# Performance work log

Hardware: AMD Instinct MI355X
Metric: run time of the kernel (lower is better)

The kernel has to match this reference:

```python
import jax, jax.numpy as jnp
import numpy as np

N_NODES = 50000
N_EDGES = 400000
NODE_DIM = 128
NUM_BASIS = 20
MUL0, MUL1, MUL2 = 128, 64, 32          # 128x0e + 64x1e + 32x2e
NUM_IRREPS = MUL0 + MUL1 + MUL2         # 224
SPH_DIM = MUL0 + 3 * MUL1 + 5 * MUL2    # 480
HIDDEN = NODE_DIM + NUM_IRREPS          # 352
EPS = 1e-5


def layer_norm(x, g, b):
    mu = x.mean(-1, keepdims=True)
    var = ((x - mu) ** 2).mean(-1, keepdims=True)
    return (x - mu) * jax.lax.rsqrt(var + EPS) * g + b


def o3_layer_norm(x, w, b):
    # Equivariant layer norm per irrep block (Equiformer-style, component normalization).
    s = x[:, :MUL0]                                    # l=0 scalars [N,128]
    v = x[:, MUL0:MUL0 + 3 * MUL1].reshape(-1, MUL1, 3)  # l=1 [N,64,3]
    t = x[:, MUL0 + 3 * MUL1:].reshape(-1, MUL2, 5)      # l=2 [N,32,5]
    s = s - s.mean(-1, keepdims=True)
    s = s * jax.lax.rsqrt((s ** 2).mean(-1, keepdims=True) + EPS) * w[:MUL0] + b
    nv = (v ** 2).mean(axis=(-1, -2))[:, None, None]
    v = v * jax.lax.rsqrt(nv + EPS) * w[MUL0:MUL0 + MUL1][None, :, None]
    nt = (t ** 2).mean(axis=(-1, -2))[:, None, None]
    t = t * jax.lax.rsqrt(nt + EPS) * w[MUL0 + MUL1:][None, :, None]
    return jnp.concatenate([s, v.reshape(-1, 3 * MUL1), t.reshape(-1, 5 * MUL2)], axis=-1)


def sph_harm(vec):
    # e3nn spherical harmonics (normalize=True, normalization='component') up to l=2.
    u = vec * jax.lax.rsqrt((vec ** 2).sum(-1, keepdims=True))
    x, y, z = u[:, 0], u[:, 1], u[:, 2]
    s15 = np.float32(np.sqrt(15.0))
    s5 = np.float32(np.sqrt(5.0))
    sh1 = np.float32(np.sqrt(3.0)) * u  # [E,3]
    sh2 = jnp.stack([s15 * x * z,
                     s15 * x * y,
                     s5 * (y * y - 0.5 * (x * x + z * z)),
                     s15 * y * z,
                     0.5 * s15 * (z * z - x * x)], axis=-1)  # [E,5]
    return sh1, sh2


def _forward(x_scalar, x_spherical, rbf, vec, W1, b1, W2, b2, Wrbf, ln_g, ln_b, o3_w, o3_b, edge_index):
    dst, src = edge_index[0], edge_index[1]
    scalar_in = layer_norm(x_scalar, ln_g, ln_b)          # [N,128]
    spherical_in = o3_layer_norm(x_spherical, o3_w, o3_b)  # [N,480]
    h = jax.nn.silu(scalar_in @ W1 + b1)
    scalar_out = h @ W2 + b2                               # [N,352]
    filter_weight = rbf @ Wrbf                             # [E,352]
    filter_out = scalar_out[src] * filter_weight           # gather + elementwise [E,352]
    gate = filter_out[:, :NUM_IRREPS]                      # [E,224]
    message_scalar = filter_out[:, NUM_IRREPS:]            # [E,128]
    sh1, sh2 = sph_harm(vec)
    g0 = gate[:, :MUL0]
    g1 = gate[:, MUL0:MUL0 + MUL1]
    g2 = gate[:, MUL0 + MUL1:]
    # ElementwiseTensorProduct(edge_irreps, '224x0e'): scalar gate per irrep; l=0 SH == 1.
    msg1 = (g1[:, :, None] * sh1[:, None, :]).reshape(-1, 3 * MUL1)
    msg2 = (g2[:, :, None] * sh2[:, None, :]).reshape(-1, 5 * MUL2)
    message_spherical = jnp.concatenate([g0, msg1, msg2], axis=-1)  # [E,480]
    new_scalar = scalar_in.at[dst].add(message_scalar)
    new_spherical = spherical_in.at[dst].add(message_spherical)
    return new_scalar, new_spherical


def setup_inputs() -> dict:
    key = jax.random.key(0)
    ks = jax.random.split(key, 8)
    return {
        "x_scalar": jax.random.normal(ks[0], (N_NODES, NODE_DIM), dtype=jnp.float32),
        "x_spherical": jax.random.normal(ks[1], (N_NODES, SPH_DIM), dtype=jnp.float32),
        "rbf": jax.random.normal(ks[2], (N_EDGES, NUM_BASIS), dtype=jnp.float32),
        "vec": jax.random.normal(ks[3], (N_EDGES, 3), dtype=jnp.float32),
        "W1": jax.random.normal(ks[4], (NODE_DIM, NODE_DIM), dtype=jnp.float32) * 0.05,
        "b1": jnp.zeros((NODE_DIM,), jnp.float32),
        "W2": jax.random.normal(ks[5], (NODE_DIM, HIDDEN), dtype=jnp.float32) * 0.05,
        "b2": jnp.zeros((HIDDEN,), jnp.float32),
        "Wrbf": jax.random.normal(ks[6], (NUM_BASIS, HIDDEN), dtype=jnp.float32) * 0.05,
        "ln_g": jnp.ones((NODE_DIM,), jnp.float32),
        "ln_b": jnp.zeros((NODE_DIM,), jnp.float32),
        "o3_w": jnp.ones((NUM_IRREPS,), jnp.float32),
        "o3_b": jnp.zeros((MUL0,), jnp.float32),
        "edge_index": jax.random.randint(ks[7], (2, N_EDGES), 0, N_NODES),
    }


def reference(x_scalar, x_spherical, rbf, vec, W1, b1, W2, b2, Wrbf, ln_g, ln_b, o3_w, o3_b, edge_index):
    return _forward(x_scalar, x_spherical, rbf, vec, W1, b1, W2, b2, Wrbf, ln_g, ln_b, o3_w, o3_b, edge_index)
```

## Files before the change

kernel.cpp:

```cpp
#include <hip/hip_runtime.h>
#include <hip/hip_bf16.h>

#define N_DIM   128
#define MUL0    128
#define MUL1    64
#define MUL2    32
#define NIRR    224
#define SPHD    480
#define HID     352
#define NBASIS  20
#define EPSV    1e-5f

typedef __attribute__((ext_vector_type(8))) short bf16x8;
typedef __attribute__((ext_vector_type(4))) float f32x4;

__device__ __forceinline__ float wave_sum(float v) {
  #pragma unroll
  for (int o = 32; o > 0; o >>= 1) v += __shfl_xor(v, o, 64);
  return v;
}

__device__ __forceinline__ unsigned short f2bf(float f) {
  unsigned int u = __float_as_uint(f);
  u = (u + 0x7fff + ((u >> 16) & 1)) >> 16;
  return (unsigned short)u;
}

__global__ __launch_bounds__(256) void node_norm_kernel(
    const float* __restrict__ x_scalar, const float* __restrict__ x_sph,
    const float* __restrict__ ln_g, const float* __restrict__ ln_b,
    const float* __restrict__ o3_w, const float* __restrict__ o3_b,
    float* __restrict__ out_scal, float* __restrict__ out_sph, int n_nodes) {
  const int n = blockIdx.x * 4 + (threadIdx.x >> 6);
  if (n >= n_nodes) return;
  const int l = threadIdx.x & 63;

  const float* xs = x_scalar + (size_t)n * N_DIM;
  float a0 = xs[l], a1 = xs[l + 64];
  float mu = wave_sum(a0 + a1) * (1.f / 128.f);
  float d0 = a0 - mu, d1 = a1 - mu;
  float var = wave_sum(d0 * d0 + d1 * d1) * (1.f / 128.f);
  float sc = rsqrtf(var + EPSV);
  float* os = out_scal + (size_t)n * N_DIM;
  os[l]      = d0 * sc * ln_g[l]      + ln_b[l];
  os[l + 64] = d1 * sc * ln_g[l + 64] + ln_b[l + 64];

  const float* xp = x_sph + (size_t)n * SPHD;
  float s0 = xp[l], s1 = xp[l + 64];
  mu = wave_sum(s0 + s1) * (1.f / 128.f);
  d0 = s0 - mu; d1 = s1 - mu;
  var = wave_sum(d0 * d0 + d1 * d1) * (1.f / 128.f);
  sc = rsqrtf(var + EPSV);
  float* op = out_sph + (size_t)n * SPHD;
  op[l]      = d0 * sc * o3_w[l]      + o3_b[l];
  op[l + 64] = d1 * sc * o3_w[l + 64] + o3_b[l + 64];

  float v0 = xp[128 + l], v1 = xp[128 + 64 + l], v2 = xp[128 + 128 + l];
  float nv = wave_sum(v0 * v0 + v1 * v1 + v2 * v2) * (1.f / 192.f);
  sc = rsqrtf(nv + EPSV);
  op[128 + l]       = v0 * sc * o3_w[MUL0 + (l) / 3];
  op[128 + 64 + l]  = v1 * sc * o3_w[MUL0 + (l + 64) / 3];
  op[128 + 128 + l] = v2 * sc * o3_w[MUL0 + (l + 128) / 3];

  float t0 = xp[320 + l], t1 = xp[320 + 64 + l];
  float t2 = (l < 32) ? xp[320 + 128 + l] : 0.f;
  float nt = wave_sum(t0 * t0 + t1 * t1 + t2 * t2) * (1.f / 160.f);
  sc = rsqrtf(nt + EPSV);
  op[320 + l]      = t0 * sc * o3_w[MUL0 + MUL1 + (l) / 5];
  op[320 + 64 + l] = t1 * sc * o3_w[MUL0 + MUL1 + (l + 64) / 5];
  if (l < 32) op[320 + 128 + l] = t2 * sc * o3_w[MUL0 + MUL1 + (l + 128) / 5];
}

__global__ void pack_b_kernel(const float* __restrict__ B, unsigned short* __restrict__ Bp,
                              int N, int NT) {
  int id = blockIdx.x * 256 + threadIdx.x;
  int total = 4 * NT * 64;
  if (id >= total) return;
  int lane = id & 63;
  int tmp = id >> 6;
  int nt = tmp % NT, ks = tmp / NT;
  int n = nt * 16 + (lane & 15);
  int kb = ks * 32 + (lane >> 4) * 8;
  unsigned short* o = Bp + (size_t)id * 8;
  #pragma unroll
  for (int j = 0; j < 8; ++j)
    o[j] = (n < N) ? f2bf(B[(size_t)(kb + j) * N + n]) : (unsigned short)0;
}

template <bool A_BF16, bool SILU, bool OUT_BF16>
__global__ __launch_bounds__(256) void mfma_gemm_kernel(
    const void* __restrict__ Ap, const unsigned short* __restrict__ Bp,
    const float* __restrict__ bias, void* __restrict__ Cp,
    int M, int N, int NT) {
  const int lane = threadIdx.x & 63;
  const int wave = threadIdx.x >> 6;
  const int bm = blockIdx.x * 64 + wave * 16;
  const int bn = blockIdx.y * 64;
  const int q = lane >> 4;
  const int arow = min(bm + (lane & 15), M - 1);

  f32x4 acc[4] = {};
  #pragma unroll
  for (int ks = 0; ks < 4; ++ks) {
    const int k = ks * 32 + q * 8;
    bf16x8 a;
    if (A_BF16) {
      a = *(const bf16x8*)((const unsigned short*)Ap + (size_t)arow * 128 + k);
    } else {
      const float* ap = (const float*)Ap + (size_t)arow * 128 + k;
      float4 f0 = *(const float4*)ap;
      float4 f1 = *(const float4*)(ap + 4);
      union { bf16x8 v; unsigned short s[8]; } cv;
      cv.s[0] = f2bf(f0.x); cv.s[1] = f2bf(f0.y); cv.s[2] = f2bf(f0.z); cv.s[3] = f2bf(f0.w);
      cv.s[4] = f2bf(f1.x); cv.s[5] = f2bf(f1.y); cv.s[6] = f2bf(f1.z); cv.s[7] = f2bf(f1.w);
      a = cv.v;
    }
    #pragma unroll
    for (int nt = 0; nt < 4; ++nt) {
      bf16x8 b = *(const bf16x8*)(Bp + ((size_t)(ks * NT + blockIdx.y * 4 + nt) * 64 + lane) * 8);
      acc[nt] = __builtin_amdgcn_mfma_f32_16x16x32_bf16(a, b, acc[nt], 0, 0, 0);
    }
  }
  #pragma unroll
  for (int nt = 0; nt < 4; ++nt) {
    int col = bn + nt * 16 + (lane & 15);
    if (col >= N) continue;
    float bz = bias[col];
    #pragma unroll
    for (int i = 0; i < 4; ++i) {
      int r = bm + q * 4 + i;
      if (r >= M) continue;
      float v = acc[nt][i] + bz;
      if (SILU) v = v / (1.f + __expf(-v));
      if (OUT_BF16) ((unsigned short*)Cp)[(size_t)r * N + col] = f2bf(v);
      else          ((float*)Cp)[(size_t)r * N + col] = v;
    }
  }
}

__global__ void hist_kernel(const int* __restrict__ ei, int* __restrict__ deg, int n_edges) {
  int e = blockIdx.x * blockDim.x + threadIdx.x;
  if (e < n_edges) atomicAdd(&deg[ei[e]], 1);
}

__global__ __launch_bounds__(1024) void scan_part_kernel(
    const int* __restrict__ deg, int* __restrict__ offs, int* __restrict__ bsum, int n) {
  __shared__ int wsum[16];
  const int tid = threadIdx.x, lane = tid & 63, wid = tid >> 6;
  int i = blockIdx.x * 1024 + tid;
  int v = (i < n) ? deg[i] : 0;
  int s = v;
  #pragma unroll
  for (int o = 1; o < 64; o <<= 1) {
    int t = __shfl_up(s, o, 64);
    if (lane >= o) s += t;
  }
  if (lane == 63) wsum[wid] = s;
  __syncthreads();
  if (wid == 0) {
    int ws = (lane < 16) ? wsum[lane] : 0;
    #pragma unroll
    for (int o = 1; o < 16; o <<= 1) {
      int t = __shfl_up(ws, o, 64);
      if (lane >= o) ws += t;
    }
    if (lane < 16) wsum[lane] = ws;
  }
  __syncthreads();
  int excl = ((wid == 0) ? 0 : wsum[wid - 1]) + s - v;
  if (i < n) offs[i] = excl;
  if (tid == 1023) bsum[blockIdx.x] = wsum[15];
}

__global__ __launch_bounds__(64) void scan_tops_kernel(
    const int* __restrict__ bsum, int* __restrict__ bbase, int* __restrict__ offs,
    int nb, int n) {
  const int lane = threadIdx.x;
  int v = (lane < nb) ? bsum[lane] : 0;
  int s = v;
  #pragma unroll
  for (int o = 1; o < 64; o <<= 1) {
    int t = __shfl_up(s, o, 64);
    if (lane >= o) s += t;
  }
  if (lane < nb) bbase[lane] = s - v;
  if (lane == 63) offs[n] = s;
}

__global__ __launch_bounds__(1024) void scan_add_kernel(
    int* __restrict__ offs, const int* __restrict__ bbase, int n) {
  int i = blockIdx.x * 1024 + threadIdx.x;
  if (i < n) offs[i] += bbase[blockIdx.x];
}

__global__ void fill_kernel(const int* __restrict__ ei, const int* __restrict__ offs,
                            int* __restrict__ cursor, int* __restrict__ sorted, int n_edges) {
  int e = blockIdx.x * blockDim.x + threadIdx.x;
  if (e < n_edges) {
    int d = ei[e];
    int p = atomicAdd(&cursor[d], 1);
    sorted[offs[d] + p] = e;
  }
}

__global__ __launch_bounds__(256) void pregather_kernel(
    const float* __restrict__ rbf, const float* __restrict__ vec,
    const int* __restrict__ edge_src, const int* __restrict__ sorted,
    float* __restrict__ rbf_s, float* __restrict__ vec_s, int* __restrict__ src_s,
    int n_edges) {
  const int i = blockIdx.x * 256 + threadIdx.x;
  const int nf4 = n_edges * 5;
  if (i < nf4) {
    int ii = i / 5, j = i - ii * 5;
    int e = sorted[ii];
    ((float4*)rbf_s)[i] = ((const float4*)rbf)[(size_t)e * 5 + j];
  }
  const int nv = n_edges * 3;
  if (i < nv) {
    int ii = i / 3, j = i - ii * 3;
    int e = sorted[ii];
    vec_s[i] = vec[(size_t)e * 3 + j];
  }
  if (i < n_edges) {
    src_s[i] = edge_src[sorted[i]];
  }
}

#define NPB 4
#define S3f  1.7320508075688772f
#define S15f 3.872983346207417f
#define S5f  2.2360679774997896f

__device__ __forceinline__ void edge_accum(
    int ii, float sA, float sB,
    const float* __restrict__ rbf_s, const float* __restrict__ vec_s,
    const float* wA, const float* wB, int t, bool hasB,
    float& a0, float& a1, float& a2, float& a3, float& a4, float& aB) {
  const float4* rp = (const float4*)(rbf_s + (size_t)ii * NBASIS);
  float4 r0 = rp[0], r1 = rp[1], r2 = rp[2], r3 = rp[3], r4 = rp[4];
  float rb[NBASIS] = {r0.x, r0.y, r0.z, r0.w, r1.x, r1.y, r1.z, r1.w,
                      r2.x, r2.y, r2.z, r2.w, r3.x, r3.y, r3.z, r3.w,
                      r4.x, r4.y, r4.z, r4.w};
  float fwA = 0.f;
  #pragma unroll
  for (int k = 0; k < NBASIS; ++k) fwA += rb[k] * wA[k];
  float fA = sA * fwA;

  if (t < 128) {
    a0 += fA;
  } else if (t < 224) {
    float vx = vec_s[3 * (size_t)ii], vy = vec_s[3 * (size_t)ii + 1], vz = vec_s[3 * (size_t)ii + 2];
    float rn = rsqrtf(vx * vx + vy * vy + vz * vz);
    float x = vx * rn, y = vy * rn, z = vz * rn;
    if (t < 192) {
      a0 += fA * (S3f * x); a1 += fA * (S3f * y); a2 += fA * (S3f * z);
    } else {
      a0 += fA * (S15f * x * z);
      a1 += fA * (S15f * x * y);
      a2 += fA * (S5f * (y * y - 0.5f * (x * x + z * z)));
      a3 += fA * (S15f * y * z);
      a4 += fA * (0.5f * S15f * (z * z - x * x));
    }
  } else {
    a0 += fA;
  }

  if (hasB) {
    float fwB = 0.f;
    #pragma unroll
    for (int k = 0; k < NBASIS; ++k) fwB += rb[k] * wB[k];
    aB += sB * fwB;
  }
}

__global__ __launch_bounds__(256) void gather_kernel(
    const float* __restrict__ rbf_s, const float* __restrict__ vec_s,
    const float* __restrict__ Wrbf, const float* __restrict__ so,
    const int* __restrict__ src_s, const int* __restrict__ offs,
    float* __restrict__ out_scal, float* __restrict__ out_sph, int n_nodes) {
  const int t = threadIdx.x;
  const bool hasB = (t < 96);
  const int cA = t;
  const int cB = hasB ? (256 + t) : 256;

  float wA[NBASIS], wB[NBASIS];
  #pragma unroll
  for (int k = 0; k < NBASIS; ++k) {
    wA[k] = Wrbf[k * HID + cA];
    wB[k] = Wrbf[k * HID + cB];
  }

  const int nb = blockIdx.x * NPB;
  for (int nn = 0; nn < NPB; ++nn) {
    const int node = nb + nn;
    if (node >= n_nodes) break;
    float accA0 = 0.f, accA1 = 0.f, accA2 = 0.f, accA3 = 0.f, accA4 = 0.f;
    float accB = 0.f;
    const int e0 = offs[node], e1 = offs[node + 1];

    int ii = e0;
    for (; ii + 2 <= e1; ii += 2) {
      const int s0 = src_s[ii], s1 = src_s[ii + 1];
      const float* p0 = so + (size_t)s0 * HID;
      const float* p1 = so + (size_t)s1 * HID;
      float sA0 = p0[cA], sA1 = p1[cA];
      float sB0 = hasB ? p0[cB] : 0.f;
      float sB1 = hasB ? p1[cB] : 0.f;
      edge_accum(ii,     sA0, sB0, rbf_s, vec_s, wA, wB, t, hasB,
                 accA0, accA1, accA2, accA3, accA4, accB);
      edge_accum(ii + 1, sA1, sB1, rbf_s, vec_s, wA, wB, t, hasB,
                 accA0, accA1, accA2, accA3, accA4, accB);
    }
    if (ii < e1) {
      const int s0 = src_s[ii];
      const float* p0 = so + (size_t)s0 * HID;
      float sA0 = p0[cA];
      float sB0 = hasB ? p0[cB] : 0.f;
      edge_accum(ii, sA0, sB0, rbf_s, vec_s, wA, wB, t, hasB,
                 accA0, accA1, accA2, accA3, accA4, accB);
    }

    float* sph = out_sph + (size_t)node * SPHD;
    float* scl = out_scal + (size_t)node * N_DIM;
    if (t < 128) {
      sph[t] += accA0;
    } else if (t < 192) {
      float* p = sph + 128 + 3 * (t - 128);
      p[0] += accA0; p[1] += accA1; p[2] += accA2;
    } else if (t < 224) {
      float* p = sph + 320 + 5 * (t - 192);
      p[0] += accA0; p[1] += accA1; p[2] += accA2; p[3] += accA3; p[4] += accA4;
    } else {
      scl[t - 224] += accA0;
    }
    if (hasB) scl[t + 32] += accB;
  }
}

extern "C" void kernel_launch(void* const* d_in, const int* in_sizes, int n_in,
                              void* d_out, int out_size, void* d_ws, size_t ws_size,
                              hipStream_t stream) {
  const float* x_scalar = (const float*)d_in[0];
  const float* x_sph    = (const float*)d_in[1];
  const float* rbf      = (const float*)d_in[2];
  const float* vec      = (const float*)d_in[3];
  const float* W1       = (const float*)d_in[4];
  const float* b1       = (const float*)d_in[5];
  const float* W2       = (const float*)d_in[6];
  const float* b2       = (const float*)d_in[7];
  const float* Wrbf     = (const float*)d_in[8];
  const float* ln_g     = (const float*)d_in[9];
  const float* ln_b     = (const float*)d_in[10];
  const float* o3_w     = (const float*)d_in[11];
  const float* o3_b     = (const float*)d_in[12];
  const int*   edge_idx = (const int*)d_in[13];

  const int n_nodes = in_sizes[0] / N_DIM;
  const int n_edges = in_sizes[2] / NBASIS;

  float* out_scal = (float*)d_out;
  float* out_sph  = out_scal + (size_t)n_nodes * N_DIM;

  float* rbf_s = (float*)d_ws;
  float* vec_s = rbf_s + (size_t)n_edges * NBASIS;
  int*   src_s = (int*)(vec_s + (size_t)n_edges * 3);
  float* ws_so = (float*)(src_s + n_edges);
  unsigned short* h_bf = (unsigned short*)(ws_so + (size_t)n_nodes * HID);
  unsigned short* bp1  = h_bf + (size_t)n_nodes * N_DIM;
  unsigned short* bp2  = bp1 + 16384;
  int* deg    = (int*)(bp2 + 49152);
  int* cursor = deg + n_nodes;
  int* offs   = cursor + n_nodes;
  int* bsum   = offs + n_nodes + 1;
  int* bbase  = bsum + 64;
  int* sorted = bbase + 64;

  const int* edge_dst = edge_idx;
  const int* edge_src = edge_idx + n_edges;

  node_norm_kernel<<<(n_nodes + 3) / 4, 256, 0, stream>>>(
      x_scalar, x_sph, ln_g, ln_b, o3_w, o3_b, out_scal, out_sph, n_nodes);

  pack_b_kernel<<<8, 256, 0, stream>>>(W1, bp1, N_DIM, 8);
  pack_b_kernel<<<24, 256, 0, stream>>>(W2, bp2, HID, 24);

  {
    dim3 g((n_nodes + 63) / 64, 2);
    mfma_gemm_kernel<false, true, true><<<g, 256, 0, stream>>>(
        out_scal, bp1, b1, h_bf, n_nodes, N_DIM, 8);
  }
  {
    dim3 g((n_nodes + 63) / 64, 6);
    mfma_gemm_kernel<true, false, false><<<g, 256, 0, stream>>>(
        h_bf, bp2, b2, ws_so, n_nodes, HID, 24);
  }

  hipMemsetAsync(deg, 0, sizeof(int) * 2 * n_nodes, stream);
  hist_kernel<<<(n_edges + 255) / 256, 256, 0, stream>>>(edge_dst, deg, n_edges);
  const int nb = (n_nodes + 1023) / 1024;
  scan_part_kernel<<<nb, 1024, 0, stream>>>(deg, offs, bsum, n_nodes);
  scan_tops_kernel<<<1, 64, 0, stream>>>(bsum, bbase, offs, nb, n_nodes);
  scan_add_kernel<<<nb, 1024, 0, stream>>>(offs, bbase, n_nodes);
  fill_kernel<<<(n_edges + 255) / 256, 256, 0, stream>>>(edge_dst, offs, cursor, sorted, n_edges);

  pregather_kernel<<<(n_edges * 5 + 255) / 256, 256, 0, stream>>>(
      rbf, vec, edge_src, sorted, rbf_s, vec_s, src_s, n_edges);

  gather_kernel<<<(n_nodes + NPB - 1) / NPB, 256, 0, stream>>>(
      rbf_s, vec_s, Wrbf, ws_so, src_s, offs, out_scal, out_sph, n_nodes);
}
```

Measured before the change: 668.9 us.

## Fuse edge pregather into CSR fill and flatten gather loop across nodes

The fill kernel now scatters src, rbf and vec directly into dst-sorted order, which removes the separate sorted index array and the pregather kernel launch. The gather kernel walks a flat edge range covering 8 nodes with 4-way unrolled source loads, flushing accumulators at node boundaries. The intent is to raise memory-level parallelism across short per-node edge lists. It also sets an occupancy hint in launch bounds. The fused scatter writes each edge's rbf row through a single thread, so rows land at random positions rather than being coalesced.

```diff
diff --git a/kernel.cpp b/kernel.cpp
--- a/kernel.cpp
+++ b/kernel.cpp
@@ -194,39 +194,26 @@
 }
 
 __global__ void fill_kernel(const int* __restrict__ ei, const int* __restrict__ offs,
-                            int* __restrict__ cursor, int* __restrict__ sorted, int n_edges) {
+                            int* __restrict__ cursor, const int* __restrict__ edge_src,
+                            const float* __restrict__ rbf, const float* __restrict__ vec,
+                            float* __restrict__ rbf_s, float* __restrict__ vec_s,
+                            int* __restrict__ src_s, int n_edges) {
   int e = blockIdx.x * blockDim.x + threadIdx.x;
   if (e < n_edges) {
     int d = ei[e];
     int p = atomicAdd(&cursor[d], 1);
-    sorted[offs[d] + p] = e;
-  }
-}
-
-__global__ __launch_bounds__(256) void pregather_kernel(
-    const float* __restrict__ rbf, const float* __restrict__ vec,
-    const int* __restrict__ edge_src, const int* __restrict__ sorted,
-    float* __restrict__ rbf_s, float* __restrict__ vec_s, int* __restrict__ src_s,
-    int n_edges) {
-  const int i = blockIdx.x * 256 + threadIdx.x;
-  const int nf4 = n_edges * 5;
-  if (i < nf4) {
-    int ii = i / 5, j = i - ii * 5;
-    int e = sorted[ii];
-    ((float4*)rbf_s)[i] = ((const float4*)rbf)[(size_t)e * 5 + j];
-  }
-  const int nv = n_edges * 3;
-  if (i < nv) {
-    int ii = i / 3, j = i - ii * 3;
-    int e = sorted[ii];
-    vec_s[i] = vec[(size_t)e * 3 + j];
-  }
-  if (i < n_edges) {
-    src_s[i] = edge_src[sorted[i]];
-  }
-}
-
-#define NPB 4
+    int ii = offs[d] + p;
+    src_s[ii] = edge_src[e];
+    const float4* rp = (const float4*)(rbf + (size_t)e * NBASIS);
+    float4* op = (float4*)(rbf_s + (size_t)ii * NBASIS);
+    op[0] = rp[0]; op[1] = rp[1]; op[2] = rp[2]; op[3] = rp[3]; op[4] = rp[4];
+    vec_s[(size_t)ii * 3]     = vec[(size_t)e * 3];
+    vec_s[(size_t)ii * 3 + 1] = vec[(size_t)e * 3 + 1];
+    vec_s[(size_t)ii * 3 + 2] = vec[(size_t)e * 3 + 2];
+  }
+}
+
+#define NPB 8
 #define S3f  1.7320508075688772f
 #define S15f 3.872983346207417f
 #define S5f  2.2360679774997896f
@@ -273,7 +260,7 @@
   }
 }
 
-__global__ __launch_bounds__(256) void gather_kernel(
+__global__ __launch_bounds__(256, 6) void gather_kernel(
     const float* __restrict__ rbf_s, const float* __restrict__ vec_s,
     const float* __restrict__ Wrbf, const float* __restrict__ so,
     const int* __restrict__ src_s, const int* __restrict__ offs,
@@ -290,51 +277,77 @@
     wB[k] = Wrbf[k * HID + cB];
   }
 
-  const int nb = blockIdx.x * NPB;
-  for (int nn = 0; nn < NPB; ++nn) {
-    const int node = nb + nn;
-    if (node >= n_nodes) break;
-    float accA0 = 0.f, accA1 = 0.f, accA2 = 0.f, accA3 = 0.f, accA4 = 0.f;
-    float accB = 0.f;
-    const int e0 = offs[node], e1 = offs[node + 1];
-
-    int ii = e0;
-    for (; ii + 2 <= e1; ii += 2) {
-      const int s0 = src_s[ii], s1 = src_s[ii + 1];
-      const float* p0 = so + (size_t)s0 * HID;
-      const float* p1 = so + (size_t)s1 * HID;
-      float sA0 = p0[cA], sA1 = p1[cA];
-      float sB0 = hasB ? p0[cB] : 0.f;
-      float sB1 = hasB ? p1[cB] : 0.f;
-      edge_accum(ii,     sA0, sB0, rbf_s, vec_s, wA, wB, t, hasB,
-                 accA0, accA1, accA2, accA3, accA4, accB);
-      edge_accum(ii + 1, sA1, sB1, rbf_s, vec_s, wA, wB, t, hasB,
-                 accA0, accA1, accA2, accA3, accA4, accB);
-    }
-    if (ii < e1) {
-      const int s0 = src_s[ii];
-      const float* p0 = so + (size_t)s0 * HID;
-      float sA0 = p0[cA];
-      float sB0 = hasB ? p0[cB] : 0.f;
-      edge_accum(ii, sA0, sB0, rbf_s, vec_s, wA, wB, t, hasB,
-                 accA0, accA1, accA2, accA3, accA4, accB);
-    }
-
+  const int n0 = blockIdx.x * NPB;
+  if (n0 >= n_nodes) return;
+  const int nE = min(n0 + NPB, n_nodes);
+
+  float a0 = 0.f, a1 = 0.f, a2 = 0.f, a3 = 0.f, a4 = 0.f, aB = 0.f;
+  bool dirty = false;
+  int cur = n0;
+  int bnd = offs[cur + 1];
+  int ii = offs[n0];
+  const int E1 = offs[nE];
+
+  auto flush = [&](int node) {
     float* sph = out_sph + (size_t)node * SPHD;
     float* scl = out_scal + (size_t)node * N_DIM;
     if (t < 128) {
-      sph[t] += accA0;
+      sph[t] += a0;
     } else if (t < 192) {
       float* p = sph + 128 + 3 * (t - 128);
-      p[0] += accA0; p[1] += accA1; p[2] += accA2;
+      p[0] += a0; p[1] += a1; p[2] += a2;
     } else if (t < 224) {
       float* p = sph + 320 + 5 * (t - 192);
-      p[0] += accA0; p[1] += accA1; p[2] += accA2; p[3] += accA3; p[4] += accA4;
+      p[0] += a0; p[1] += a1; p[2] += a2; p[3] += a3; p[4] += a4;
     } else {
-      scl[t - 224] += accA0;
-    }
-    if (hasB) scl[t + 32] += accB;
-  }
+      scl[t - 224] += a0;
+    }
+    if (hasB) scl[t + 32] += aB;
+    a0 = a1 = a2 = a3 = a4 = aB = 0.f;
+  };
+
+  #define ADVANCE()                                               \
+    while (ii >= bnd) {                                           \
+      if (dirty) { flush(cur); dirty = false; }                   \
+      ++cur; bnd = offs[cur + 1];                                 \
+    }
+
+  while (ii + 4 <= E1) {
+    const int s0 = src_s[ii], s1 = src_s[ii + 1], s2 = src_s[ii + 2], s3 = src_s[ii + 3];
+    const float* p0 = so + (size_t)s0 * HID;
+    const float* p1 = so + (size_t)s1 * HID;
+    const float* p2 = so + (size_t)s2 * HID;
+    const float* p3 = so + (size_t)s3 * HID;
+    float sA0 = p0[cA], sA1 = p1[cA], sA2 = p2[cA], sA3 = p3[cA];
+    float sB0 = hasB ? p0[cB] : 0.f;
+    float sB1 = hasB ? p1[cB] : 0.f;
+    float sB2 = hasB ? p2[cB] : 0.f;
+    float sB3 = hasB ? p3[cB] : 0.f;
+
+    ADVANCE();
+    edge_accum(ii, sA0, sB0, rbf_s, vec_s, wA, wB, t, hasB, a0, a1, a2, a3, a4, aB);
+    dirty = true; ++ii;
+    ADVANCE();
+    edge_accum(ii, sA1, sB1, rbf_s, vec_s, wA, wB, t, hasB, a0, a1, a2, a3, a4, aB);
+    dirty = true; ++ii;
+    ADVANCE();
+    edge_accum(ii, sA2, sB2, rbf_s, vec_s, wA, wB, t, hasB, a0, a1, a2, a3, a4, aB);
+    dirty = true; ++ii;
+    ADVANCE();
+    edge_accum(ii, sA3, sB3, rbf_s, vec_s, wA, wB, t, hasB, a0, a1, a2, a3, a4, aB);
+    dirty = true; ++ii;
+  }
+  while (ii < E1) {
+    const int s0 = src_s[ii];
+    const float* p0 = so + (size_t)s0 * HID;
+    float sA0 = p0[cA];
+    float sB0 = hasB ? p0[cB] : 0.f;
+    ADVANCE();
+    edge_accum(ii, sA0, sB0, rbf_s, vec_s, wA, wB, t, hasB, a0, a1, a2, a3, a4, aB);
+    dirty = true; ++ii;
+  }
+  if (dirty) flush(cur);
+  #undef ADVANCE
 }
 
 extern "C" void kernel_launch(void* const* d_in, const int* in_sizes, int n_in,
@@ -373,7 +386,6 @@
   int* offs   = cursor + n_nodes;
   int* bsum   = offs + n_nodes + 1;
   int* bbase  = bsum + 64;
-  int* sorted = bbase + 64;
 
   const int* edge_dst = edge_idx;
   const int* edge_src = edge_idx + n_edges;
@@ -401,10 +413,8 @@
   scan_part_kernel<<<nb, 1024, 0, stream>>>(deg, offs, bsum, n_nodes);
   scan_tops_kernel<<<1, 64, 0, stream>>>(bsum, bbase, offs, nb, n_nodes);
   scan_add_kernel<<<nb, 1024, 0, stream>>>(offs, bbase, n_nodes);
-  fill_kernel<<<(n_edges + 255) / 256, 256, 0, stream>>>(edge_dst, offs, cursor, sorted, n_edges);
-
-  pregather_kernel<<<(n_edges * 5 + 255) / 256, 256, 0, stream>>>(
-      rbf, vec, edge_src, sorted, rbf_s, vec_s, src_s, n_edges);
+  fill_kernel<<<(n_edges + 255) / 256, 256, 0, stream>>>(
+      edge_dst, offs, cursor, edge_src, rbf, vec, rbf_s, vec_s, src_s, n_edges);
 
   gather_kernel<<<(n_nodes + NPB - 1) / NPB, 256, 0, stream>>>(
       rbf_s, vec_s, Wrbf, ws_so, src_s, offs, out_scal, out_sph, n_nodes);
```

Result: slower. 691.1 us (+3.3%).
